# Kernel tuning notes

Measured on AMD Instinct MI355X. Metric: run time of the kernel, lower is better.

The kernel has to match this reference:

```python
import jax, jax.numpy as jnp
import numpy as np

TOP_K = 2
EPS = 1e-9


def setup_inputs() -> dict:
    key = jax.random.key(0)
    k1, k2, k3 = jax.random.split(key, 3)
    B, S, D, E = 8, 4096, 1024, 8
    x = jax.random.normal(k1, (B, S, D), dtype=jnp.float32)
    W = jax.random.normal(k2, (E, D), dtype=jnp.float32) / np.sqrt(D).astype(np.float32)
    noise = jax.random.uniform(k3, (B, S, E), dtype=jnp.float32)
    return {"x": x, "W": W, "noise": noise}


def reference(x, W, noise):
    E = W.shape[0]  # num routed experts; total experts = E + 1
    # gate logits: [B, S, E]
    logits = jnp.einsum('bsd,ed->bse', x, W)
    gumbel = -jnp.log(-jnp.log(noise + EPS) + EPS)
    scores = jax.nn.softmax(logits + gumbel, axis=-1)
    # top-k routing
    topk_scores, topk_idx = jax.lax.top_k(scores, TOP_K)  # [B, S, K]
    # scatter into dispatch mask over E+1 slots (slot 0 is the shared expert)
    onehot = jax.nn.one_hot(topk_idx + 1, E + 1, dtype=scores.dtype)  # [B, S, K, E+1]
    dispatch_mask = jnp.einsum('bske,bsk->bse', onehot, topk_scores)
    dispatch_mask = dispatch_mask.at[..., 0].set(1.0)
    # load-balance auxiliary loss
    me = scores.mean(axis=(0, 1))
    ce = (scores ** 2).mean(axis=(0, 1))
    load_balance_loss = (me * ce).sum() * (E ** 2)
    return dispatch_mask, load_balance_loss
```

## Files before the change

kernel.cpp:

```cpp
#include <hip/hip_runtime.h>
#include <math.h>

#define NEXP 8
#define DIM 1024
#define NTOK 32768
#define EPSF 1e-9f

#define K1_NB 2048
#define K2_NB 512

__global__ __launch_bounds__(256, 4) void logits_kernel(
    const float* __restrict__ x, const float* __restrict__ W,
    float* __restrict__ out)
{
    __shared__ float4 Wlds[NEXP * DIM / 4];

    const int tid  = threadIdx.x;
    const int lane = tid & 63;
    const int wid  = tid >> 6;

    const float4* Wg = (const float4*)W;
    #pragma unroll
    for (int i = 0; i < (NEXP * DIM / 4) / 256; ++i)
        Wlds[tid + i * 256] = Wg[tid + i * 256];
    __syncthreads();

    const int gw = (blockIdx.x << 2) + wid;
    const int t0 = gw << 2;

    const bool p0 = lane & 1;
    const bool p1 = (lane >> 1) & 1;
    const bool p2 = (lane >> 2) & 1;

    #pragma unroll
    for (int half = 0; half < 2; ++half) {
        const int ta = t0 + half * 2;

        float4 xv[2][4];
        #pragma unroll
        for (int j = 0; j < 2; ++j)
            #pragma unroll
            for (int p = 0; p < 4; ++p)
                xv[j][p] = *(const float4*)(x + (size_t)(ta + j) * DIM + p * 256 + (lane << 2));

        float acc[2][NEXP];
        #pragma unroll
        for (int j = 0; j < 2; ++j)
            #pragma unroll
            for (int e = 0; e < NEXP; ++e) acc[j][e] = 0.f;

        #pragma unroll
        for (int p = 0; p < 4; ++p)
            #pragma unroll
            for (int e = 0; e < NEXP; ++e) {
                float4 wv = Wlds[e * 256 + p * 64 + lane];
                #pragma unroll
                for (int j = 0; j < 2; ++j)
                    acc[j][e] += xv[j][p].x * wv.x + xv[j][p].y * wv.y
                               + xv[j][p].z * wv.z + xv[j][p].w * wv.w;
            }

        float k4[2][4];
        #pragma unroll
        for (int j = 0; j < 2; ++j)
            #pragma unroll
            for (int k = 0; k < 4; ++k) {
                float a = acc[j][2 * k], b = acc[j][2 * k + 1];
                float keep = p0 ? b : a, give = p0 ? a : b;
                k4[j][k] = keep + __shfl_xor(give, 1);
            }
        float k2v[2][2];
        #pragma unroll
        for (int j = 0; j < 2; ++j)
            #pragma unroll
            for (int k = 0; k < 2; ++k) {
                float a = k4[j][2 * k], b = k4[j][2 * k + 1];
                float keep = p1 ? b : a, give = p1 ? a : b;
                k2v[j][k] = keep + __shfl_xor(give, 2);
            }
        float z[2];
        #pragma unroll
        for (int j = 0; j < 2; ++j) {
            float a = k2v[j][0], b = k2v[j][1];
            float keep = p2 ? b : a, give = p2 ? a : b;
            z[j] = keep + __shfl_xor(give, 4);
        }
        #pragma unroll
        for (int j = 0; j < 2; ++j) {
            z[j] += __shfl_xor(z[j], 8);
            z[j] += __shfl_xor(z[j], 16);
            z[j] += __shfl_xor(z[j], 32);
        }

        if (lane < 16) {
            int j = lane >> 3, e = lane & 7;
            out[(size_t)(ta + j) * 9 + 1 + e] = j ? z[1] : z[0];
        }
    }
}

__global__ __launch_bounds__(64) void epilogue_kernel(
    const float* __restrict__ noise, float* __restrict__ out,
    float* __restrict__ partials)
{
    const int lane = threadIdx.x;
    const int t = blockIdx.x * 64 + lane;

    float z[NEXP];
    #pragma unroll
    for (int e = 0; e < NEXP; ++e)
        z[e] = out[(size_t)t * 9 + 1 + e];

    float4 n0 = *(const float4*)(noise + (size_t)t * NEXP);
    float4 n1 = *(const float4*)(noise + (size_t)t * NEXP + 4);
    float nv[NEXP] = {n0.x, n0.y, n0.z, n0.w, n1.x, n1.y, n1.z, n1.w};

    #pragma unroll
    for (int e = 0; e < NEXP; ++e)
        z[e] += -logf(-logf(nv[e] + EPSF) + EPSF);

    float m = z[0];
    #pragma unroll
    for (int e = 1; e < NEXP; ++e) m = fmaxf(m, z[e]);

    float sc[NEXP], s = 0.f;
    #pragma unroll
    for (int e = 0; e < NEXP; ++e) { sc[e] = expf(z[e] - m); s += sc[e]; }
    float inv = 1.0f / s;
    #pragma unroll
    for (int e = 0; e < NEXP; ++e) sc[e] *= inv;

    float b1v = sc[0]; int b1i = 0;
    float b2v = -1.f;  int b2i = -1;
    #pragma unroll
    for (int e = 1; e < NEXP; ++e) {
        if (sc[e] > b1v)      { b2v = b1v; b2i = b1i; b1v = sc[e]; b1i = e; }
        else if (sc[e] > b2v) { b2v = sc[e]; b2i = e; }
    }

    out[(size_t)t * 9] = 1.0f;
    #pragma unroll
    for (int e = 0; e < NEXP; ++e)
        out[(size_t)t * 9 + 1 + e] = (e == b1i) ? b1v : (e == b2i) ? b2v : 0.f;

    float v[16];
    #pragma unroll
    for (int e = 0; e < NEXP; ++e) { v[e] = sc[e]; v[8 + e] = sc[e] * sc[e]; }
    #pragma unroll
    for (int d = 1; d < 64; d <<= 1)
        #pragma unroll
        for (int k = 0; k < 16; ++k)
            v[k] += __shfl_xor(v[k], d);

    if (lane == 0) {
        #pragma unroll
        for (int k = 0; k < 16; ++k)
            partials[blockIdx.x * 16 + k] = v[k];
    }
}

__global__ __launch_bounds__(64) void finalize_kernel(
    const float* __restrict__ partials, float* __restrict__ out)
{
    const int lane = threadIdx.x;
    const int v = lane & 15, rg = lane >> 4;

    float a4[4] = {0.f, 0.f, 0.f, 0.f};
    #pragma unroll
    for (int i = 0; i < K2_NB / 16; ++i)
        #pragma unroll
        for (int q = 0; q < 4; ++q)
            a4[q] += partials[((i * 4 + q) * 4 + rg) * 16 + v];
    float s = (a4[0] + a4[1]) + (a4[2] + a4[3]);

    s += __shfl_xor(s, 16);
    s += __shfl_xor(s, 32);

    const float invN = 1.0f / (float)NTOK;
    float partner = __shfl_xor(s, 8);
    float prod = (s * invN) * (partner * invN);
    prod += __shfl_xor(prod, 1);
    prod += __shfl_xor(prod, 2);
    prod += __shfl_xor(prod, 4);
    if (lane == 0)
        out[(size_t)NTOK * 9] = prod * 64.0f;
}

extern "C" void kernel_launch(void* const* d_in, const int* in_sizes, int n_in,
                              void* d_out, int out_size, void* d_ws, size_t ws_size,
                              hipStream_t stream) {
    const float* x     = (const float*)d_in[0];
    const float* W     = (const float*)d_in[1];
    const float* noise = (const float*)d_in[2];
    float* out = (float*)d_out;
    float* partials = (float*)d_ws;

    logits_kernel<<<K1_NB, 256, 0, stream>>>(x, W, out);
    epilogue_kernel<<<K2_NB, 64, 0, stream>>>(noise, out, partials);
    finalize_kernel<<<1, 64, 0, stream>>>(partials, out);
}
```

Baseline: 36.50 us.

## Fuse gumbel-softmax/top-k epilogue into logits kernel via LDS

```diff
diff --git a/kernel.cpp b/kernel.cpp
--- a/kernel.cpp
+++ b/kernel.cpp
@@ -6,14 +6,16 @@
 #define NTOK 32768
 #define EPSF 1e-9f
 
-#define K1_NB 2048
-#define K2_NB 512
-
-__global__ __launch_bounds__(256, 4) void logits_kernel(
+#define K1_NB 1024
+
+__global__ __launch_bounds__(256, 4) void fused_kernel(
     const float* __restrict__ x, const float* __restrict__ W,
-    float* __restrict__ out)
+    const float* __restrict__ noise, float* __restrict__ out,
+    float* __restrict__ partials)
 {
     __shared__ float4 Wlds[NEXP * DIM / 4];
+    __shared__ float  zlds[4][8][8];
+    __shared__ float  slds[4][8][16];
 
     const int tid  = threadIdx.x;
     const int lane = tid & 63;
@@ -26,15 +28,15 @@
     __syncthreads();
 
     const int gw = (blockIdx.x << 2) + wid;
-    const int t0 = gw << 2;
+    const int t0 = gw << 3;
 
     const bool p0 = lane & 1;
     const bool p1 = (lane >> 1) & 1;
     const bool p2 = (lane >> 2) & 1;
 
     #pragma unroll
-    for (int half = 0; half < 2; ++half) {
-        const int ta = t0 + half * 2;
+    for (int h = 0; h < 4; ++h) {
+        const int ta = t0 + h * 2;
 
         float4 xv[2][4];
         #pragma unroll
@@ -92,98 +94,98 @@
             z[j] += __shfl_xor(z[j], 32);
         }
 
-        if (lane < 16) {
-            int j = lane >> 3, e = lane & 7;
-            out[(size_t)(ta + j) * 9 + 1 + e] = j ? z[1] : z[0];
+        if (lane < 16)
+            zlds[wid][h * 2 + (lane >> 3)][lane & 7] = (lane >> 3) ? z[1] : z[0];
+    }
+
+    __syncthreads();
+
+    if (lane < 8) {
+        const int t = t0 + lane;
+
+        float4 za = *(const float4*)&zlds[wid][lane][0];
+        float4 zb = *(const float4*)&zlds[wid][lane][4];
+        float zt[NEXP] = {za.x, za.y, za.z, za.w, zb.x, zb.y, zb.z, zb.w};
+
+        float4 n0 = *(const float4*)(noise + (size_t)t * NEXP);
+        float4 n1 = *(const float4*)(noise + (size_t)t * NEXP + 4);
+        float nv[NEXP] = {n0.x, n0.y, n0.z, n0.w, n1.x, n1.y, n1.z, n1.w};
+
+        #pragma unroll
+        for (int e = 0; e < NEXP; ++e)
+            zt[e] += -logf(-logf(nv[e] + EPSF) + EPSF);
+
+        float m = zt[0];
+        #pragma unroll
+        for (int e = 1; e < NEXP; ++e) m = fmaxf(m, zt[e]);
+
+        float sc[NEXP], s = 0.f;
+        #pragma unroll
+        for (int e = 0; e < NEXP; ++e) { sc[e] = expf(zt[e] - m); s += sc[e]; }
+        float inv = 1.0f / s;
+        #pragma unroll
+        for (int e = 0; e < NEXP; ++e) sc[e] *= inv;
+
+        float b1v = sc[0]; int b1i = 0;
+        float b2v = -1.f;  int b2i = -1;
+        #pragma unroll
+        for (int e = 1; e < NEXP; ++e) {
+            if (sc[e] > b1v)      { b2v = b1v; b2i = b1i; b1v = sc[e]; b1i = e; }
+            else if (sc[e] > b2v) { b2v = sc[e]; b2i = e; }
         }
+
+        out[(size_t)t * 9] = 1.0f;
+        #pragma unroll
+        for (int e = 0; e < NEXP; ++e)
+            out[(size_t)t * 9 + 1 + e] = (e == b1i) ? b1v : (e == b2i) ? b2v : 0.f;
+
+        *(float4*)&slds[wid][lane][0]  = make_float4(sc[0], sc[1], sc[2], sc[3]);
+        *(float4*)&slds[wid][lane][4]  = make_float4(sc[4], sc[5], sc[6], sc[7]);
+        *(float4*)&slds[wid][lane][8]  = make_float4(sc[0]*sc[0], sc[1]*sc[1], sc[2]*sc[2], sc[3]*sc[3]);
+        *(float4*)&slds[wid][lane][12] = make_float4(sc[4]*sc[4], sc[5]*sc[5], sc[6]*sc[6], sc[7]*sc[7]);
+    }
+
+    __syncthreads();
+    if (tid < 16) {
+        float s = 0.f;
+        #pragma unroll
+        for (int w = 0; w < 4; ++w)
+            #pragma unroll
+            for (int j = 0; j < 8; ++j)
+                s += slds[w][j][tid];
+        partials[blockIdx.x * 16 + tid] = s;
     }
 }
 
-__global__ __launch_bounds__(64) void epilogue_kernel(
-    const float* __restrict__ noise, float* __restrict__ out,
-    float* __restrict__ partials)
-{
-    const int lane = threadIdx.x;
-    const int t = blockIdx.x * 64 + lane;
-
-    float z[NEXP];
-    #pragma unroll
-    for (int e = 0; e < NEXP; ++e)
-        z[e] = out[(size_t)t * 9 + 1 + e];
-
-    float4 n0 = *(const float4*)(noise + (size_t)t * NEXP);
-    float4 n1 = *(const float4*)(noise + (size_t)t * NEXP + 4);
-    float nv[NEXP] = {n0.x, n0.y, n0.z, n0.w, n1.x, n1.y, n1.z, n1.w};
-
-    #pragma unroll
-    for (int e = 0; e < NEXP; ++e)
-        z[e] += -logf(-logf(nv[e] + EPSF) + EPSF);
-
-    float m = z[0];
-    #pragma unroll
-    for (int e = 1; e < NEXP; ++e) m = fmaxf(m, z[e]);
-
-    float sc[NEXP], s = 0.f;
-    #pragma unroll
-    for (int e = 0; e < NEXP; ++e) { sc[e] = expf(z[e] - m); s += sc[e]; }
-    float inv = 1.0f / s;
-    #pragma unroll
-    for (int e = 0; e < NEXP; ++e) sc[e] *= inv;
-
-    float b1v = sc[0]; int b1i = 0;
-    float b2v = -1.f;  int b2i = -1;
-    #pragma unroll
-    for (int e = 1; e < NEXP; ++e) {
-        if (sc[e] > b1v)      { b2v = b1v; b2i = b1i; b1v = sc[e]; b1i = e; }
-        else if (sc[e] > b2v) { b2v = sc[e]; b2i = e; }
-    }
-
-    out[(size_t)t * 9] = 1.0f;
-    #pragma unroll
-    for (int e = 0; e < NEXP; ++e)
-        out[(size_t)t * 9 + 1 + e] = (e == b1i) ? b1v : (e == b2i) ? b2v : 0.f;
-
-    float v[16];
-    #pragma unroll
-    for (int e = 0; e < NEXP; ++e) { v[e] = sc[e]; v[8 + e] = sc[e] * sc[e]; }
-    #pragma unroll
-    for (int d = 1; d < 64; d <<= 1)
-        #pragma unroll
-        for (int k = 0; k < 16; ++k)
-            v[k] += __shfl_xor(v[k], d);
-
-    if (lane == 0) {
-        #pragma unroll
-        for (int k = 0; k < 16; ++k)
-            partials[blockIdx.x * 16 + k] = v[k];
-    }
-}
-
-__global__ __launch_bounds__(64) void finalize_kernel(
+__global__ __launch_bounds__(256) void finalize_kernel(
     const float* __restrict__ partials, float* __restrict__ out)
 {
-    const int lane = threadIdx.x;
-    const int v = lane & 15, rg = lane >> 4;
+    __shared__ float lds16[16][16];
+    const int tid = threadIdx.x;
+    const int v = tid & 15, rg = tid >> 4;
 
     float a4[4] = {0.f, 0.f, 0.f, 0.f};
     #pragma unroll
-    for (int i = 0; i < K2_NB / 16; ++i)
+    for (int i = 0; i < K1_NB / 64; ++i)
         #pragma unroll
         for (int q = 0; q < 4; ++q)
-            a4[q] += partials[((i * 4 + q) * 4 + rg) * 16 + v];
-    float s = (a4[0] + a4[1]) + (a4[2] + a4[3]);
-
-    s += __shfl_xor(s, 16);
-    s += __shfl_xor(s, 32);
-
-    const float invN = 1.0f / (float)NTOK;
-    float partner = __shfl_xor(s, 8);
-    float prod = (s * invN) * (partner * invN);
-    prod += __shfl_xor(prod, 1);
-    prod += __shfl_xor(prod, 2);
-    prod += __shfl_xor(prod, 4);
-    if (lane == 0)
-        out[(size_t)NTOK * 9] = prod * 64.0f;
+            a4[q] += partials[((i * 4 + q) * 16 + rg) * 16 + v];
+    lds16[rg][v] = (a4[0] + a4[1]) + (a4[2] + a4[3]);
+
+    __syncthreads();
+    if (tid < 16) {
+        float tot = 0.f;
+        #pragma unroll
+        for (int g = 0; g < 16; ++g) tot += lds16[g][tid];
+        const float invN = 1.0f / (float)NTOK;
+        float partner = __shfl_xor(tot, 8);
+        float prod = (tot * invN) * (partner * invN);
+        prod += __shfl_xor(prod, 1);
+        prod += __shfl_xor(prod, 2);
+        prod += __shfl_xor(prod, 4);
+        if (tid == 0)
+            out[(size_t)NTOK * 9] = prod * 64.0f;
+    }
 }
 
 extern "C" void kernel_launch(void* const* d_in, const int* in_sizes, int n_in,
@@ -195,7 +197,6 @@
     float* out = (float*)d_out;
     float* partials = (float*)d_ws;
 
-    logits_kernel<<<K1_NB, 256, 0, stream>>>(x, W, out);
-    epilogue_kernel<<<K2_NB, 64, 0, stream>>>(noise, out, partials);
-    finalize_kernel<<<1, 64, 0, stream>>>(partials, out);
+    fused_kernel<<<K1_NB, 256, 0, stream>>>(x, W, noise, out, partials);
+    finalize_kernel<<<1, 256, 0, stream>>>(partials, out);
 }
```

After: 35.56 us. -2.6%, faster.
